# Performance work log

Hardware: AMD Instinct MI355X
Metric: run time of the kernel (lower is better)

Reference implementation:

```python
import jax, jax.numpy as jnp
import numpy as np

B, T, J, D = 1024, 128, 5, 64
H = 128            # GRU hidden
HEADS, HD = 4, 32  # GAT heads / head dim
GAT_OUT = HEADS * HD
MID, OUT, P = 128, 64, 4
NEG_SLOPE = 0.2


def setup_inputs() -> dict:
    key = jax.random.key(0)
    ks = jax.random.split(key, 20)
    s = 0.05
    obs = jax.random.normal(ks[0], (B, T, J, D), jnp.float32)
    # fixed bidirectional 5-node chain (as in _make_chain_edge_index)
    src = list(range(J - 1)) + list(range(1, J))
    dst = list(range(1, J)) + list(range(J - 1))
    edge_index = jnp.array([src, dst], dtype=jnp.int32)  # [2, 8]
    p = {
        # GRU (torch layout: gates ordered r, z, n)
        'W_ih': jax.random.normal(ks[1], (3 * H, D)) * s,
        'W_hh': jax.random.normal(ks[2], (3 * H, H)) * s,
        'b_ih': jax.random.normal(ks[3], (3 * H,)) * s,
        'b_hh': jax.random.normal(ks[4], (3 * H,)) * s,
        # GATConv
        'gat_W': jax.random.normal(ks[5], (H, GAT_OUT)) * s,
        'att_src': jax.random.normal(ks[6], (HEADS, HD)) * s,
        'att_dst': jax.random.normal(ks[7], (HEADS, HD)) * s,
        'gat_b': jax.random.normal(ks[8], (GAT_OUT,)) * s,
        # trunk MLP
        'W1': jax.random.normal(ks[9], (GAT_OUT, MID)) * s,
        'b1': jax.random.normal(ks[10], (MID,)) * s,
        'W2': jax.random.normal(ks[11], (MID, OUT)) * s,
        'b2': jax.random.normal(ks[12], (OUT,)) * s,
        # 5 actor heads stacked + critic
        'actor_W': jax.random.normal(ks[13], (J, OUT, P)) * s,
        'actor_b': jax.random.normal(ks[14], (J, P)) * s,
        'critic_W': jax.random.normal(ks[15], (OUT, 1)) * s,
        'critic_b': jax.random.normal(ks[16], (1,)) * s,
    }
    return {'obs': obs, 'edge_index': edge_index, **p}


def _forward(obs, edge_index, W_ih, W_hh, b_ih, b_hh, gat_W, att_src, att_dst,
             gat_b, W1, b1, W2, b2, actor_W, actor_b, critic_W, critic_b):
    Bb, Tt, Jj, Dd = obs.shape
    # temporal encoder: one GRU shared across junctions, batch = B*J
    x = obs.transpose(0, 2, 1, 3).reshape(Bb * Jj, Tt, Dd)

    def step(h, xt):
        gi = xt @ W_ih.T + b_ih            # [BJ, 3H]
        gh = h @ W_hh.T + b_hh
        i_r, i_z, i_n = jnp.split(gi, 3, axis=-1)
        h_r, h_z, h_n = jnp.split(gh, 3, axis=-1)
        r = jax.nn.sigmoid(i_r + h_r)
        z = jax.nn.sigmoid(i_z + h_z)
        n = jnp.tanh(i_n + r * h_n)
        return (1.0 - z) * n + z * h, None

    h0 = jnp.zeros((Bb * Jj, H), obs.dtype)
    hT, _ = jax.lax.scan(step, h0, x.transpose(1, 0, 2))  # final hidden [BJ, H]
    h = hT.reshape(Bb, Jj, H)

    # GATConv over the fixed 5-node chain, done densely per batch graph.
    # PyG semantics: edge (src -> dst), self-loops added, softmax over incoming
    # edges per dst node, messages are transformed src features.
    xp = (h @ gat_W).reshape(Bb, Jj, HEADS, HD)
    a_s = jnp.einsum('bjhd,hd->bjh', xp, att_src)  # per-src score
    a_d = jnp.einsum('bihd,hd->bih', xp, att_dst)  # per-dst score
    e = a_s[:, None, :, :] + a_d[:, :, None, :]    # [B, dst_i, src_j, heads]
    e = jax.nn.leaky_relu(e, NEG_SLOPE)
    adj = jnp.zeros((Jj, Jj), bool).at[edge_index[1], edge_index[0]].set(True)
    adj = adj | jnp.eye(Jj, dtype=bool)            # add self-loops
    e = jnp.where(adj[None, :, :, None], e, -jnp.inf)
    alpha = jax.nn.softmax(e, axis=2)              # softmax over src j per dst i
    g = jnp.einsum('bijh,bjhd->bihd', alpha, xp).reshape(Bb, Jj, GAT_OUT) + gat_b

    # shared trunk MLP
    t = jax.nn.relu(jax.nn.relu(g @ W1 + b1) @ W2 + b2)  # [B, J, OUT]

    # per-junction actor heads + critic on junction-mean
    logits = jnp.einsum('bjo,jop->bjp', t, actor_W) + actor_b  # [B, J, P]
    value = t.mean(axis=1) @ critic_W + critic_b               # [B, 1]
    return logits, value


def reference(obs, edge_index, W_ih, W_hh, b_ih, b_hh, gat_W, att_src, att_dst,
              gat_b, W1, b1, W2, b2, actor_W, actor_b, critic_W, critic_b):
    return _forward(obs, edge_index, W_ih, W_hh, b_ih, b_hh, gat_W, att_src,
                    att_dst, gat_b, W1, b1, W2, b2, actor_W, actor_b,
                    critic_W, critic_b)
```

## Files before the change

### kernel.cpp

```cpp
#include <hip/hip_runtime.h>
#include <hip/hip_bf16.h>

typedef short shortx4 __attribute__((ext_vector_type(4)));
typedef short short8 __attribute__((ext_vector_type(8)));
typedef float floatx4 __attribute__((ext_vector_type(4)));

#define MFMA_BF16(A, B, C) __builtin_amdgcn_mfma_f32_16x16x32_bf16((A), (B), (C), 0, 0, 0)
#define LOG2E 1.44269504088896340736f

__device__ __forceinline__ float bf2f(const __hip_bfloat16 v) { return __bfloat162float(v); }

__device__ __forceinline__ unsigned rne_bits(float f) {
    unsigned u = __builtin_bit_cast(unsigned, f);
    return u + 0x7fffu + ((u >> 16) & 1u);
}
__device__ __forceinline__ unsigned pack_bf16(float a, float b) {
    return (rne_bits(b) & 0xffff0000u) | (rne_bits(a) >> 16);
}
__device__ __forceinline__ short bf16_s(float f) { return (short)(rne_bits(f) >> 16); }

__device__ __forceinline__ short8 cvt8(const float4 a, const float4 b) {
    union { unsigned u[4]; short8 s; } r;
    r.u[0] = pack_bf16(a.x, a.y);
    r.u[1] = pack_bf16(a.z, a.w);
    r.u[2] = pack_bf16(b.x, b.y);
    r.u[3] = pack_bf16(b.z, b.w);
    return r.s;
}

__device__ __forceinline__ short8 ld_s8(const short* p) {
    union { struct { shortx4 lo, hi; } p; short8 v; } u;
    u.p.lo = *reinterpret_cast<const shortx4*>(p);
    u.p.hi = *reinterpret_cast<const shortx4*>(p + 4);
    return u.v;
}

__device__ __forceinline__ float fast_sigmoid(float x) {
    const float e = __builtin_amdgcn_exp2f(-x * LOG2E);
    return __builtin_amdgcn_rcpf(1.0f + e);
}
__device__ __forceinline__ float fast_tanh(float x) {
    const float e = __builtin_amdgcn_exp2f(x * (2.0f * LOG2E));
    return 1.0f - 2.0f * __builtin_amdgcn_rcpf(e + 1.0f);
}

__global__ __launch_bounds__(512) void gru_kernel(
    const float* __restrict__ obs,
    const float* __restrict__ W_ih,
    const float* __restrict__ W_hh,
    const float* __restrict__ b_ih,
    const float* __restrict__ b_hh,
    __hip_bfloat16* __restrict__ h_out)
{
    __shared__ alignas(16) short h_lds[2 * 16 * 132];
    __shared__ alignas(16) short x_lds[2 * 16 * 68];

    const int tid = threadIdx.x;
    const int w = tid >> 6;
    const int lane = tid & 63;
    const int q = lane >> 4;
    const int c = lane & 15;
    const int r0 = blockIdx.x * 16;

    for (int i = tid; i < 2 * 16 * 132; i += 512) h_lds[i] = 0;

    short8 wih[3][2];
    short8 whh[3][4];
#pragma unroll
    for (int g = 0; g < 3; ++g) {
        const int col = g * 128 + w * 16 + c;
#pragma unroll
        for (int f = 0; f < 2; ++f) {
            const float4 a = *reinterpret_cast<const float4*>(W_ih + col * 64 + f * 32 + q * 8);
            const float4 b = *reinterpret_cast<const float4*>(W_ih + col * 64 + f * 32 + q * 8 + 4);
            wih[g][f] = cvt8(a, b);
        }
#pragma unroll
        for (int f = 0; f < 4; ++f) {
            const float4 a = *reinterpret_cast<const float4*>(W_hh + col * 128 + f * 32 + q * 8);
            const float4 b = *reinterpret_cast<const float4*>(W_hh + col * 128 + f * 32 + q * 8 + 4);
            whh[g][f] = cvt8(a, b);
        }
    }

    const int cc = w * 16 + c;
    const float br_ = b_ih[cc] + b_hh[cc];
    const float bz_ = b_ih[128 + cc] + b_hh[128 + cc];
    const float bin_ = b_ih[256 + cc];
    const float bhn_ = b_hh[256 + cc];
    const floatx4 cbias_r  = {br_, br_, br_, br_};
    const floatx4 cbias_z  = {bz_, bz_, bz_, bz_};
    const floatx4 cbias_in = {bin_, bin_, bin_, bin_};
    const floatx4 cbias_hn = {bhn_, bhn_, bhn_, bhn_};

    const int srow = tid >> 5, scp = tid & 31;
    {
        const int rs = r0 + srow;
        const int bbs = rs / 5;
        const int jjs = rs - bbs * 5;
        const float* xgs = obs + bbs * 40960 + jjs * 64 + scp * 2;
        unsigned* xb32 = reinterpret_cast<unsigned*>(x_lds);
        const float2 v0 = *reinterpret_cast<const float2*>(xgs);
        xb32[srow * 34 + scp] = pack_bf16(v0.x, v0.y);
        float2 vn = *reinterpret_cast<const float2*>(xgs + 320);

        float h_keep[4] = {0.0f, 0.0f, 0.0f, 0.0f};

        __syncthreads();

        int bufo = 0;
        for (int t = 0; t < 128; ++t) {
            const int nbufo = 2112 - bufo;
            const short* hb = &h_lds[bufo];
            const short* xb = &x_lds[(t & 1) * 1088];

            const short8 xc0 = ld_s8(xb + c * 68 + q * 8);
            const short8 xc1 = ld_s8(xb + c * 68 + 32 + q * 8);
            short8 hf[4];
#pragma unroll
            for (int f = 0; f < 4; ++f)
                hf[f] = ld_s8(hb + c * 132 + f * 32 + q * 8);

            unsigned* xw = reinterpret_cast<unsigned*>(&x_lds[((t + 1) & 1) * 1088]);
            xw[srow * 34 + scp] = pack_bf16(vn.x, vn.y);
            const int tp = (t + 2) > 127 ? 127 : (t + 2);
            vn = *reinterpret_cast<const float2*>(xgs + tp * 320);

            floatx4 ar  = MFMA_BF16(xc0, wih[0][0], cbias_r);
            floatx4 az  = MFMA_BF16(xc0, wih[1][0], cbias_z);
            floatx4 ain = MFMA_BF16(xc0, wih[2][0], cbias_in);
            ar  = MFMA_BF16(xc1, wih[0][1], ar);
            az  = MFMA_BF16(xc1, wih[1][1], az);
            ain = MFMA_BF16(xc1, wih[2][1], ain);
            floatx4 ahn = MFMA_BF16(hf[0], whh[2][0], cbias_hn);
#pragma unroll
            for (int f = 0; f < 4; ++f) {
                ar = MFMA_BF16(hf[f], whh[0][f], ar);
                az = MFMA_BF16(hf[f], whh[1][f], az);
                if (f > 0) ahn = MFMA_BF16(hf[f], whh[2][f], ahn);
            }

            short* hnb = &h_lds[nbufo];
#pragma unroll
            for (int i = 0; i < 4; ++i) {
                const float rr = fast_sigmoid(ar[i]);
                const float zz = fast_sigmoid(az[i]);
                const float nn = fast_tanh(ain[i] + rr * ahn[i]);
                const float hv = nn + zz * (h_keep[i] - nn);
                h_keep[i] = hv;
                hnb[(4 * q + i) * 132 + w * 16 + c] = bf16_s(hv);
            }

            bufo = nbufo;
            __syncthreads();
        }

#pragma unroll
        for (int i = 0; i < 4; ++i)
            h_out[(r0 + 4 * q + i) * 128 + w * 16 + c] = __float2bfloat16(h_keep[i]);
    }
}

__global__ __launch_bounds__(256) void head_kernel(
    const __hip_bfloat16* __restrict__ h_in,
    const float* __restrict__ gat_W,
    const float* __restrict__ att_src,
    const float* __restrict__ att_dst,
    const float* __restrict__ gat_b,
    const float* __restrict__ W1,
    const float* __restrict__ b1,
    const float* __restrict__ W2,
    const float* __restrict__ b2,
    const float* __restrict__ actor_W,
    const float* __restrict__ actor_b,
    const float* __restrict__ critic_W,
    const float* __restrict__ critic_b,
    float* __restrict__ out)
{
    __shared__ float hs[5][128];
    __shared__ float xp[5][128];
    __shared__ float gs[5][128];
    __shared__ float t1[5][128];
    __shared__ float t2[5][64];
    __shared__ float pp[1280];
    __shared__ float as_[5][4];
    __shared__ float ad_[5][4];

    const int tid = threadIdx.x;
    const int b = blockIdx.x;

    for (int i = tid; i < 640; i += 256)
        hs[i >> 7][i & 127] = bf2f(h_in[b * 640 + i]);
    __syncthreads();

    {
        const int kh = tid >> 7, col = tid & 127;
        float acc[5] = {0, 0, 0, 0, 0};
#pragma unroll 8
        for (int k2 = 0; k2 < 64; ++k2) {
            const int k = kh * 64 + k2;
            const float wv = gat_W[k * 128 + col];
#pragma unroll
            for (int i = 0; i < 5; ++i) acc[i] += hs[i][k] * wv;
        }
#pragma unroll
        for (int i = 0; i < 5; ++i) pp[kh * 640 + i * 128 + col] = acc[i];
    }
    __syncthreads();
    for (int i = tid; i < 640; i += 256)
        xp[i >> 7][i & 127] = pp[i] + pp[640 + i];
    __syncthreads();

    if (tid < 40) {
        const int row = tid >> 3;
        const int hd = (tid >> 1) & 3;
        const int which = tid & 1;
        const float* att = which ? att_dst : att_src;
        float acc = 0.0f;
#pragma unroll
        for (int d = 0; d < 32; ++d) acc += xp[row][hd * 32 + d] * att[hd * 32 + d];
        if (which) ad_[row][hd] = acc; else as_[row][hd] = acc;
    }
    __syncthreads();

    for (int i = tid; i < 640; i += 256) {
        const int dst = i >> 7, col = i & 127, hd = col >> 5;
        const float adv = ad_[dst][hd];
        float ev[3]; int js[3]; int cnt = 0; float mx = -1e30f;
#pragma unroll
        for (int dj = -1; dj <= 1; ++dj) {
            const int j = dst + dj;
            if (j < 0 || j >= 5) continue;
            float e = as_[j][hd] + adv;
            e = e > 0.0f ? e : 0.2f * e;
            js[cnt] = j; ev[cnt] = e; mx = fmaxf(mx, e); ++cnt;
        }
        float s = 0.0f, num = 0.0f;
        for (int k = 0; k < cnt; ++k) {
            const float a = __builtin_amdgcn_exp2f((ev[k] - mx) * LOG2E);
            s += a; num += a * xp[js[k]][col];
        }
        gs[dst][col] = num * __builtin_amdgcn_rcpf(s) + gat_b[col];
    }
    __syncthreads();

    {
        const int kh = tid >> 7, col = tid & 127;
        float acc[5] = {0, 0, 0, 0, 0};
#pragma unroll 8
        for (int k2 = 0; k2 < 64; ++k2) {
            const int k = kh * 64 + k2;
            const float wv = W1[k * 128 + col];
#pragma unroll
            for (int i = 0; i < 5; ++i) acc[i] += gs[i][k] * wv;
        }
#pragma unroll
        for (int i = 0; i < 5; ++i) pp[kh * 640 + i * 128 + col] = acc[i];
    }
    __syncthreads();
    for (int i = tid; i < 640; i += 256)
        t1[i >> 7][i & 127] = fmaxf(pp[i] + pp[640 + i] + b1[i & 127], 0.0f);
    __syncthreads();

    {
        const int kq = tid >> 6, col = tid & 63;
        float acc[5] = {0, 0, 0, 0, 0};
#pragma unroll 8
        for (int k2 = 0; k2 < 32; ++k2) {
            const int k = kq * 32 + k2;
            const float wv = W2[k * 64 + col];
#pragma unroll
            for (int i = 0; i < 5; ++i) acc[i] += t1[i][k] * wv;
        }
#pragma unroll
        for (int i = 0; i < 5; ++i) pp[kq * 320 + i * 64 + col] = acc[i];
    }
    __syncthreads();
    for (int i = tid; i < 320; i += 256) {
        const int row = i >> 6, col = i & 63;
        t2[row][col] = fmaxf(pp[i] + pp[320 + i] + pp[640 + i] + pp[960 + i] + b2[col], 0.0f);
    }
    __syncthreads();

    if (tid < 20) {
        const int row = tid >> 2, p = tid & 3;
        float acc = actor_b[row * 4 + p];
#pragma unroll
        for (int o = 0; o < 64; ++o)
            acc += t2[row][o] * actor_W[row * 256 + o * 4 + p];
        out[(b * 5 + row) * 4 + p] = acc;
    }
    if (tid == 64) {
        float acc = 0.0f;
#pragma unroll
        for (int o = 0; o < 64; ++o) {
            float m = 0.0f;
#pragma unroll
            for (int j = 0; j < 5; ++j) m += t2[j][o];
            acc += (m * 0.2f) * critic_W[o];
        }
        out[20480 + b] = acc + critic_b[0];
    }
}

extern "C" void kernel_launch(void* const* d_in, const int* in_sizes, int n_in,
                              void* d_out, int out_size, void* d_ws, size_t ws_size,
                              hipStream_t stream) {
    (void)in_sizes; (void)n_in; (void)out_size; (void)ws_size;
    const float* obs      = (const float*)d_in[0];
    const float* W_ih     = (const float*)d_in[2];
    const float* W_hh     = (const float*)d_in[3];
    const float* b_ih     = (const float*)d_in[4];
    const float* b_hh     = (const float*)d_in[5];
    const float* gat_W    = (const float*)d_in[6];
    const float* att_src  = (const float*)d_in[7];
    const float* att_dst  = (const float*)d_in[8];
    const float* gat_b    = (const float*)d_in[9];
    const float* W1       = (const float*)d_in[10];
    const float* b1       = (const float*)d_in[11];
    const float* W2       = (const float*)d_in[12];
    const float* b2       = (const float*)d_in[13];
    const float* actor_W  = (const float*)d_in[14];
    const float* actor_b  = (const float*)d_in[15];
    const float* critic_W = (const float*)d_in[16];
    const float* critic_b = (const float*)d_in[17];

    __hip_bfloat16* h_ws = (__hip_bfloat16*)d_ws;

    gru_kernel<<<320, 512, 0, stream>>>(obs, W_ih, W_hh, b_ih, b_hh, h_ws);
    head_kernel<<<1024, 256, 0, stream>>>(h_ws, gat_W, att_src, att_dst, gat_b,
                                          W1, b1, W2, b2, actor_W, actor_b,
                                          critic_W, critic_b,
                                          (float*)d_out);
}
```

Baseline: 428.7 us.

## Split GRU MFMA accumulation chains and deepen obs prefetch in recurrent loop

The per-step gate accumulations are split into two independent MFMA chains per gate, summed at the end, which shortens the serial dependency through the MFMA pipeline. The global prefetch of obs is deepened from one to two steps ahead so load latency is covered across more iterations. The __syncthreads is replaced by an explicit lgkmcnt wait plus s_barrier wrapped in sched_barriers, which skips the vmcnt drain so outstanding global loads can stay in flight across the barrier. In exchange there are extra vector adds and more live registers, and the sched_barriers restrict how the compiler can reorder code.

Result: slower. 484.4 us (+13.0%).

```diff
diff --git a/kernel.cpp b/kernel.cpp
--- a/kernel.cpp
+++ b/kernel.cpp
@@ -94,71 +94,88 @@
     const floatx4 cbias_hn = {bhn_, bhn_, bhn_, bhn_};
 
     const int srow = tid >> 5, scp = tid & 31;
-    {
-        const int rs = r0 + srow;
-        const int bbs = rs / 5;
-        const int jjs = rs - bbs * 5;
-        const float* xgs = obs + bbs * 40960 + jjs * 64 + scp * 2;
-        unsigned* xb32 = reinterpret_cast<unsigned*>(x_lds);
-        const float2 v0 = *reinterpret_cast<const float2*>(xgs);
-        xb32[srow * 34 + scp] = pack_bf16(v0.x, v0.y);
-        float2 vn = *reinterpret_cast<const float2*>(xgs + 320);
-
-        float h_keep[4] = {0.0f, 0.0f, 0.0f, 0.0f};
-
-        __syncthreads();
-
-        int bufo = 0;
-        for (int t = 0; t < 128; ++t) {
-            const int nbufo = 2112 - bufo;
-            const short* hb = &h_lds[bufo];
-            const short* xb = &x_lds[(t & 1) * 1088];
-
-            const short8 xc0 = ld_s8(xb + c * 68 + q * 8);
-            const short8 xc1 = ld_s8(xb + c * 68 + 32 + q * 8);
-            short8 hf[4];
-#pragma unroll
-            for (int f = 0; f < 4; ++f)
-                hf[f] = ld_s8(hb + c * 132 + f * 32 + q * 8);
-
-            unsigned* xw = reinterpret_cast<unsigned*>(&x_lds[((t + 1) & 1) * 1088]);
-            xw[srow * 34 + scp] = pack_bf16(vn.x, vn.y);
-            const int tp = (t + 2) > 127 ? 127 : (t + 2);
-            vn = *reinterpret_cast<const float2*>(xgs + tp * 320);
-
-            floatx4 ar  = MFMA_BF16(xc0, wih[0][0], cbias_r);
-            floatx4 az  = MFMA_BF16(xc0, wih[1][0], cbias_z);
-            floatx4 ain = MFMA_BF16(xc0, wih[2][0], cbias_in);
-            ar  = MFMA_BF16(xc1, wih[0][1], ar);
-            az  = MFMA_BF16(xc1, wih[1][1], az);
-            ain = MFMA_BF16(xc1, wih[2][1], ain);
-            floatx4 ahn = MFMA_BF16(hf[0], whh[2][0], cbias_hn);
-#pragma unroll
-            for (int f = 0; f < 4; ++f) {
-                ar = MFMA_BF16(hf[f], whh[0][f], ar);
-                az = MFMA_BF16(hf[f], whh[1][f], az);
-                if (f > 0) ahn = MFMA_BF16(hf[f], whh[2][f], ahn);
-            }
-
-            short* hnb = &h_lds[nbufo];
-#pragma unroll
-            for (int i = 0; i < 4; ++i) {
-                const float rr = fast_sigmoid(ar[i]);
-                const float zz = fast_sigmoid(az[i]);
-                const float nn = fast_tanh(ain[i] + rr * ahn[i]);
-                const float hv = nn + zz * (h_keep[i] - nn);
-                h_keep[i] = hv;
-                hnb[(4 * q + i) * 132 + w * 16 + c] = bf16_s(hv);
-            }
-
-            bufo = nbufo;
-            __syncthreads();
-        }
-
-#pragma unroll
-        for (int i = 0; i < 4; ++i)
-            h_out[(r0 + 4 * q + i) * 128 + w * 16 + c] = __float2bfloat16(h_keep[i]);
-    }
+    const int rs = r0 + srow;
+    const int bbs = rs / 5;
+    const int jjs = rs - bbs * 5;
+    const float* xgs = obs + bbs * 40960 + jjs * 64 + scp * 2;
+    unsigned* xb32 = reinterpret_cast<unsigned*>(x_lds);
+
+    const float2 v0 = *reinterpret_cast<const float2*>(xgs);
+    xb32[srow * 34 + scp] = pack_bf16(v0.x, v0.y);
+    float2 vnA = *reinterpret_cast<const float2*>(xgs + 320);
+    float2 vnB = *reinterpret_cast<const float2*>(xgs + 640);
+
+    float h_keep[4] = {0.0f, 0.0f, 0.0f, 0.0f};
+
+    __syncthreads();
+
+    int bufo = 0;
+    for (int t = 0; t < 128; ++t) {
+        const int nbufo = 2112 - bufo;
+        const short* hb = &h_lds[bufo];
+        const short* xb = &x_lds[(t & 1) * 1088];
+
+        const short8 xc0 = ld_s8(xb + c * 68 + q * 8);
+        const short8 xc1 = ld_s8(xb + c * 68 + 32 + q * 8);
+        short8 hf[4];
+#pragma unroll
+        for (int f = 0; f < 4; ++f)
+            hf[f] = ld_s8(hb + c * 132 + f * 32 + q * 8);
+
+        unsigned* xw = reinterpret_cast<unsigned*>(&x_lds[((t + 1) & 1) * 1088]);
+        xw[srow * 34 + scp] = pack_bf16(vnA.x, vnA.y);
+        vnA = vnB;
+        const int tp = (t + 3 > 127) ? 127 : (t + 3);
+        vnB = *reinterpret_cast<const float2*>(xgs + tp * 320);
+
+        const floatx4 z4 = {0.0f, 0.0f, 0.0f, 0.0f};
+        floatx4 arA = MFMA_BF16(xc0, wih[0][0], cbias_r);
+        floatx4 azA = MFMA_BF16(xc0, wih[1][0], cbias_z);
+        floatx4 ain = MFMA_BF16(xc0, wih[2][0], cbias_in);
+        floatx4 arB = MFMA_BF16(xc1, wih[0][1], z4);
+        floatx4 azB = MFMA_BF16(xc1, wih[1][1], z4);
+        ain = MFMA_BF16(xc1, wih[2][1], ain);
+
+        floatx4 ahnA = MFMA_BF16(hf[0], whh[2][0], cbias_hn);
+        arA = MFMA_BF16(hf[0], whh[0][0], arA);
+        azA = MFMA_BF16(hf[0], whh[1][0], azA);
+        arA = MFMA_BF16(hf[1], whh[0][1], arA);
+        azA = MFMA_BF16(hf[1], whh[1][1], azA);
+        ahnA = MFMA_BF16(hf[1], whh[2][1], ahnA);
+
+        floatx4 ahnB = MFMA_BF16(hf[2], whh[2][2], z4);
+        arB = MFMA_BF16(hf[2], whh[0][2], arB);
+        azB = MFMA_BF16(hf[2], whh[1][2], azB);
+        arB = MFMA_BF16(hf[3], whh[0][3], arB);
+        azB = MFMA_BF16(hf[3], whh[1][3], azB);
+        ahnB = MFMA_BF16(hf[3], whh[2][3], ahnB);
+
+        const floatx4 ar  = arA + arB;
+        const floatx4 az  = azA + azB;
+        const floatx4 ahn = ahnA + ahnB;
+
+        short* hnb = &h_lds[nbufo];
+#pragma unroll
+        for (int i = 0; i < 4; ++i) {
+            const float rr = fast_sigmoid(ar[i]);
+            const float zz = fast_sigmoid(az[i]);
+            const float nn = fast_tanh(ain[i] + rr * ahn[i]);
+            const float hv = nn + zz * (h_keep[i] - nn);
+            h_keep[i] = hv;
+            hnb[(4 * q + i) * 132 + w * 16 + c] = bf16_s(hv);
+        }
+
+        bufo = nbufo;
+
+        __builtin_amdgcn_sched_barrier(0);
+        asm volatile("s_waitcnt lgkmcnt(0)" ::: "memory");
+        __builtin_amdgcn_s_barrier();
+        __builtin_amdgcn_sched_barrier(0);
+    }
+
+#pragma unroll
+    for (int i = 0; i < 4; ++i)
+        h_out[(r0 + 4 * q + i) * 128 + w * 16 + c] = __float2bfloat16(h_keep[i]);
 }
 
 __global__ __launch_bounds__(256) void head_kernel(
```

## Repartition GRU to 10-row blocks of 4 waves, each wave covering 32 hidden columns

Applied to the files above, without the earlier changes.

The GRU kernel now uses 256-thread blocks, each processing 10 sequence rows instead of 16, so 512 blocks are launched instead of 320 and every CU gets work. Each wave owns 32 hidden columns, written as two interleaved MFMA column tiles, which doubles the MFMAs per wave but halves the waves per block. The M=16 MFMA tiles are now only 10/16 utilised, and the serial per-step chain per wave gets longer, in exchange for better occupancy spread across the GPU's CUs.

Result: slower. 472.1 us (+10.1%).

```diff
diff --git a/kernel.cpp b/kernel.cpp
--- a/kernel.cpp
+++ b/kernel.cpp
@@ -17,7 +17,6 @@
 __device__ __forceinline__ unsigned pack_bf16(float a, float b) {
     return (rne_bits(b) & 0xffff0000u) | (rne_bits(a) >> 16);
 }
-__device__ __forceinline__ short bf16_s(float f) { return (short)(rne_bits(f) >> 16); }
 
 __device__ __forceinline__ short8 cvt8(const float4 a, const float4 b) {
     union { unsigned u[4]; short8 s; } r;
@@ -44,7 +43,7 @@
     return 1.0f - 2.0f * __builtin_amdgcn_rcpf(e + 1.0f);
 }
 
-__global__ __launch_bounds__(512) void gru_kernel(
+__global__ __launch_bounds__(256, 2) void gru_kernel(
     const float* __restrict__ obs,
     const float* __restrict__ W_ih,
     const float* __restrict__ W_hh,
@@ -60,104 +59,144 @@
     const int lane = tid & 63;
     const int q = lane >> 4;
     const int c = lane & 15;
-    const int r0 = blockIdx.x * 16;
-
-    for (int i = tid; i < 2 * 16 * 132; i += 512) h_lds[i] = 0;
-
-    short8 wih[3][2];
-    short8 whh[3][4];
+    const int r0 = blockIdx.x * 10;
+
+    for (int i = tid; i < 2 * 16 * 132; i += 256) h_lds[i] = 0;
+    for (int i = tid; i < 2 * 16 * 68; i += 256) x_lds[i] = 0;
+
+    short8 wih[3][2][2];
+    short8 whh[3][2][4];
 #pragma unroll
     for (int g = 0; g < 3; ++g) {
-        const int col = g * 128 + w * 16 + c;
-#pragma unroll
-        for (int f = 0; f < 2; ++f) {
-            const float4 a = *reinterpret_cast<const float4*>(W_ih + col * 64 + f * 32 + q * 8);
-            const float4 b = *reinterpret_cast<const float4*>(W_ih + col * 64 + f * 32 + q * 8 + 4);
-            wih[g][f] = cvt8(a, b);
-        }
-#pragma unroll
-        for (int f = 0; f < 4; ++f) {
-            const float4 a = *reinterpret_cast<const float4*>(W_hh + col * 128 + f * 32 + q * 8);
-            const float4 b = *reinterpret_cast<const float4*>(W_hh + col * 128 + f * 32 + q * 8 + 4);
-            whh[g][f] = cvt8(a, b);
-        }
-    }
-
-    const int cc = w * 16 + c;
-    const float br_ = b_ih[cc] + b_hh[cc];
-    const float bz_ = b_ih[128 + cc] + b_hh[128 + cc];
-    const float bin_ = b_ih[256 + cc];
-    const float bhn_ = b_hh[256 + cc];
-    const floatx4 cbias_r  = {br_, br_, br_, br_};
-    const floatx4 cbias_z  = {bz_, bz_, bz_, bz_};
-    const floatx4 cbias_in = {bin_, bin_, bin_, bin_};
-    const floatx4 cbias_hn = {bhn_, bhn_, bhn_, bhn_};
-
-    const int srow = tid >> 5, scp = tid & 31;
-    {
+#pragma unroll
+        for (int ct = 0; ct < 2; ++ct) {
+            const int col = g * 128 + w * 32 + 2 * c + ct;
+#pragma unroll
+            for (int f = 0; f < 2; ++f) {
+                const float4 a = *reinterpret_cast<const float4*>(W_ih + col * 64 + f * 32 + q * 8);
+                const float4 b = *reinterpret_cast<const float4*>(W_ih + col * 64 + f * 32 + q * 8 + 4);
+                wih[g][ct][f] = cvt8(a, b);
+            }
+#pragma unroll
+            for (int f = 0; f < 4; ++f) {
+                const float4 a = *reinterpret_cast<const float4*>(W_hh + col * 128 + f * 32 + q * 8);
+                const float4 b = *reinterpret_cast<const float4*>(W_hh + col * 128 + f * 32 + q * 8 + 4);
+                whh[g][ct][f] = cvt8(a, b);
+            }
+        }
+    }
+
+    const int c0 = w * 32 + 2 * c, c1 = c0 + 1;
+    const float br0_ = b_ih[c0] + b_hh[c0];
+    const float br1_ = b_ih[c1] + b_hh[c1];
+    const float bz0_ = b_ih[128 + c0] + b_hh[128 + c0];
+    const float bz1_ = b_ih[128 + c1] + b_hh[128 + c1];
+    const float bn0_ = b_ih[256 + c0];
+    const float bn1_ = b_ih[256 + c1];
+    const float bh0_ = b_hh[256 + c0];
+    const float bh1_ = b_hh[256 + c1];
+    const floatx4 cbr0 = {br0_, br0_, br0_, br0_};
+    const floatx4 cbr1 = {br1_, br1_, br1_, br1_};
+    const floatx4 cbz0 = {bz0_, bz0_, bz0_, bz0_};
+    const floatx4 cbz1 = {bz1_, bz1_, bz1_, bz1_};
+    const floatx4 cbn0 = {bn0_, bn0_, bn0_, bn0_};
+    const floatx4 cbn1 = {bn1_, bn1_, bn1_, bn1_};
+    const floatx4 cbh0 = {bh0_, bh0_, bh0_, bh0_};
+    const floatx4 cbh1 = {bh1_, bh1_, bh1_, bh1_};
+
+    const int srow = tid >> 4, sc = tid & 15;
+    const bool stager = (tid < 160);
+    const float* xgs = nullptr;
+    float4 vn;
+    if (stager) {
         const int rs = r0 + srow;
         const int bbs = rs / 5;
         const int jjs = rs - bbs * 5;
-        const float* xgs = obs + bbs * 40960 + jjs * 64 + scp * 2;
-        unsigned* xb32 = reinterpret_cast<unsigned*>(x_lds);
-        const float2 v0 = *reinterpret_cast<const float2*>(xgs);
-        xb32[srow * 34 + scp] = pack_bf16(v0.x, v0.y);
-        float2 vn = *reinterpret_cast<const float2*>(xgs + 320);
-
-        float h_keep[4] = {0.0f, 0.0f, 0.0f, 0.0f};
-
+        xgs = obs + bbs * 40960 + jjs * 64 + sc * 4;
+        const float4 v0 = *reinterpret_cast<const float4*>(xgs);
+        uint2* xw = reinterpret_cast<uint2*>(&x_lds[srow * 68 + sc * 4]);
+        *xw = uint2{pack_bf16(v0.x, v0.y), pack_bf16(v0.z, v0.w)};
+        vn = *reinterpret_cast<const float4*>(xgs + 320);
+    }
+
+    float hk0[4] = {0.0f, 0.0f, 0.0f, 0.0f};
+    float hk1[4] = {0.0f, 0.0f, 0.0f, 0.0f};
+
+    __syncthreads();
+
+    int bufo = 0;
+    for (int t = 0; t < 128; ++t) {
+        const int nbufo = 2112 - bufo;
+        const short* hb = &h_lds[bufo];
+        const short* xb = &x_lds[(t & 1) * 1088];
+
+        const short8 xc0 = ld_s8(xb + c * 68 + q * 8);
+        const short8 xc1 = ld_s8(xb + c * 68 + 32 + q * 8);
+        short8 hf[4];
+#pragma unroll
+        for (int f = 0; f < 4; ++f)
+            hf[f] = ld_s8(hb + c * 132 + f * 32 + q * 8);
+
+        if (stager) {
+            uint2* xw = reinterpret_cast<uint2*>(&x_lds[((t + 1) & 1) * 1088 + srow * 68 + sc * 4]);
+            *xw = uint2{pack_bf16(vn.x, vn.y), pack_bf16(vn.z, vn.w)};
+            const int tp = (t + 2) > 127 ? 127 : (t + 2);
+            vn = *reinterpret_cast<const float4*>(xgs + tp * 320);
+        }
+
+        floatx4 ar0 = MFMA_BF16(xc0, wih[0][0][0], cbr0);
+        floatx4 ar1 = MFMA_BF16(xc0, wih[0][1][0], cbr1);
+        floatx4 az0 = MFMA_BF16(xc0, wih[1][0][0], cbz0);
+        floatx4 az1 = MFMA_BF16(xc0, wih[1][1][0], cbz1);
+        floatx4 an0 = MFMA_BF16(xc0, wih[2][0][0], cbn0);
+        floatx4 an1 = MFMA_BF16(xc0, wih[2][1][0], cbn1);
+        ar0 = MFMA_BF16(xc1, wih[0][0][1], ar0);
+        ar1 = MFMA_BF16(xc1, wih[0][1][1], ar1);
+        az0 = MFMA_BF16(xc1, wih[1][0][1], az0);
+        az1 = MFMA_BF16(xc1, wih[1][1][1], az1);
+        an0 = MFMA_BF16(xc1, wih[2][0][1], an0);
+        an1 = MFMA_BF16(xc1, wih[2][1][1], an1);
+
+        floatx4 ah0 = MFMA_BF16(hf[0], whh[2][0][0], cbh0);
+        floatx4 ah1 = MFMA_BF16(hf[0], whh[2][1][0], cbh1);
+#pragma unroll
+        for (int f = 0; f < 4; ++f) {
+            ar0 = MFMA_BF16(hf[f], whh[0][0][f], ar0);
+            ar1 = MFMA_BF16(hf[f], whh[0][1][f], ar1);
+            az0 = MFMA_BF16(hf[f], whh[1][0][f], az0);
+            az1 = MFMA_BF16(hf[f], whh[1][1][f], az1);
+            if (f > 0) {
+                ah0 = MFMA_BF16(hf[f], whh[2][0][f], ah0);
+                ah1 = MFMA_BF16(hf[f], whh[2][1][f], ah1);
+            }
+        }
+
+        unsigned* hw = reinterpret_cast<unsigned*>(&h_lds[nbufo]);
+#pragma unroll
+        for (int i = 0; i < 4; ++i) {
+            const float rr0 = fast_sigmoid(ar0[i]);
+            const float rr1 = fast_sigmoid(ar1[i]);
+            const float zz0 = fast_sigmoid(az0[i]);
+            const float zz1 = fast_sigmoid(az1[i]);
+            const float nn0 = fast_tanh(an0[i] + rr0 * ah0[i]);
+            const float nn1 = fast_tanh(an1[i] + rr1 * ah1[i]);
+            const float hv0 = nn0 + zz0 * (hk0[i] - nn0);
+            const float hv1 = nn1 + zz1 * (hk1[i] - nn1);
+            hk0[i] = hv0;
+            hk1[i] = hv1;
+            hw[(4 * q + i) * 66 + w * 16 + c] = pack_bf16(hv0, hv1);
+        }
+
+        bufo = nbufo;
         __syncthreads();
-
-        int bufo = 0;
-        for (int t = 0; t < 128; ++t) {
-            const int nbufo = 2112 - bufo;
-            const short* hb = &h_lds[bufo];
-            const short* xb = &x_lds[(t & 1) * 1088];
-
-            const short8 xc0 = ld_s8(xb + c * 68 + q * 8);
-            const short8 xc1 = ld_s8(xb + c * 68 + 32 + q * 8);
-            short8 hf[4];
-#pragma unroll
-            for (int f = 0; f < 4; ++f)
-                hf[f] = ld_s8(hb + c * 132 + f * 32 + q * 8);
-
-            unsigned* xw = reinterpret_cast<unsigned*>(&x_lds[((t + 1) & 1) * 1088]);
-            xw[srow * 34 + scp] = pack_bf16(vn.x, vn.y);
-            const int tp = (t + 2) > 127 ? 127 : (t + 2);
-            vn = *reinterpret_cast<const float2*>(xgs + tp * 320);
-
-            floatx4 ar  = MFMA_BF16(xc0, wih[0][0], cbias_r);
-            floatx4 az  = MFMA_BF16(xc0, wih[1][0], cbias_z);
-            floatx4 ain = MFMA_BF16(xc0, wih[2][0], cbias_in);
-            ar  = MFMA_BF16(xc1, wih[0][1], ar);
-            az  = MFMA_BF16(xc1, wih[1][1], az);
-            ain = MFMA_BF16(xc1, wih[2][1], ain);
-            floatx4 ahn = MFMA_BF16(hf[0], whh[2][0], cbias_hn);
-#pragma unroll
-            for (int f = 0; f < 4; ++f) {
-                ar = MFMA_BF16(hf[f], whh[0][f], ar);
-                az = MFMA_BF16(hf[f], whh[1][f], az);
-                if (f > 0) ahn = MFMA_BF16(hf[f], whh[2][f], ahn);
-            }
-
-            short* hnb = &h_lds[nbufo];
-#pragma unroll
-            for (int i = 0; i < 4; ++i) {
-                const float rr = fast_sigmoid(ar[i]);
-                const float zz = fast_sigmoid(az[i]);
-                const float nn = fast_tanh(ain[i] + rr * ahn[i]);
-                const float hv = nn + zz * (h_keep[i] - nn);
-                h_keep[i] = hv;
-                hnb[(4 * q + i) * 132 + w * 16 + c] = bf16_s(hv);
-            }
-
-            bufo = nbufo;
-            __syncthreads();
-        }
-
-#pragma unroll
-        for (int i = 0; i < 4; ++i)
-            h_out[(r0 + 4 * q + i) * 128 + w * 16 + c] = __float2bfloat16(h_keep[i]);
+    }
+
+    unsigned* ho = reinterpret_cast<unsigned*>(h_out);
+#pragma unroll
+    for (int i = 0; i < 4; ++i) {
+        const int row = 4 * q + i;
+        if (row < 10)
+            ho[(r0 + row) * 64 + w * 16 + c] = pack_bf16(hk0[i], hk1[i]);
     }
 }
 
@@ -327,7 +366,7 @@
 
     __hip_bfloat16* h_ws = (__hip_bfloat16*)d_ws;
 
-    gru_kernel<<<320, 512, 0, stream>>>(obs, W_ih, W_hh, b_ih, b_hh, h_ws);
+    gru_kernel<<<512, 256, 0, stream>>>(obs, W_ih, W_hh, b_ih, b_hh, h_ws);
     head_kernel<<<1024, 256, 0, stream>>>(h_ws, gat_W, att_src, att_dst, gat_b,
                                           W1, b1, W2, b2, actor_W, actor_b,
                                           critic_W, critic_b,
```

## Rebalance GRU blocks so mixed one- and two-tile blocks fill every CU

Applied to the files above, without the earlier changes.

The GRU kernel becomes a templated body that processes one or two 16-row tiles per block. Launch drops from 320 to 256 blocks: 192 blocks take one tile and 64 blocks take two, so each CU gets one block instead of some CUs running a second round. The two-tile blocks interleave independent MFMA chains to hide the recurrence latency, at the cost of more registers and LDS and a longer per-step critical path in those blocks.

New measurement: 432.1 us. No clear change (+0.8%).

```diff
diff --git a/kernel.cpp b/kernel.cpp
--- a/kernel.cpp
+++ b/kernel.cpp
@@ -44,25 +44,27 @@
     return 1.0f - 2.0f * __builtin_amdgcn_rcpf(e + 1.0f);
 }
 
-__global__ __launch_bounds__(512) void gru_kernel(
+template<int NT>
+__device__ __forceinline__ void gru_body(
+    const int r0,
     const float* __restrict__ obs,
     const float* __restrict__ W_ih,
     const float* __restrict__ W_hh,
     const float* __restrict__ b_ih,
     const float* __restrict__ b_hh,
-    __hip_bfloat16* __restrict__ h_out)
+    __hip_bfloat16* __restrict__ h_out,
+    short* h_lds, short* x_lds)
 {
-    __shared__ alignas(16) short h_lds[2 * 16 * 132];
-    __shared__ alignas(16) short x_lds[2 * 16 * 68];
-
     const int tid = threadIdx.x;
     const int w = tid >> 6;
     const int lane = tid & 63;
     const int q = lane >> 4;
     const int c = lane & 15;
-    const int r0 = blockIdx.x * 16;
-
-    for (int i = tid; i < 2 * 16 * 132; i += 512) h_lds[i] = 0;
+
+    constexpr int HBUF = NT * 16 * 132;
+    constexpr int XBUF = NT * 16 * 68;
+
+    for (int i = tid; i < 2 * HBUF; i += 512) h_lds[i] = 0;
 
     short8 wih[3][2];
     short8 whh[3][4];
@@ -93,72 +95,132 @@
     const floatx4 cbias_in = {bin_, bin_, bin_, bin_};
     const floatx4 cbias_hn = {bhn_, bhn_, bhn_, bhn_};
 
-    const int srow = tid >> 5, scp = tid & 31;
+    int srow, scw;
+    const float* xgs;
+    float2 vn2;
+    float4 vn4;
+    if constexpr (NT == 1) {
+        srow = tid >> 5; scw = tid & 31;
+    } else {
+        srow = tid >> 4; scw = tid & 15;
+    }
     {
         const int rs = r0 + srow;
         const int bbs = rs / 5;
         const int jjs = rs - bbs * 5;
-        const float* xgs = obs + bbs * 40960 + jjs * 64 + scp * 2;
-        unsigned* xb32 = reinterpret_cast<unsigned*>(x_lds);
-        const float2 v0 = *reinterpret_cast<const float2*>(xgs);
-        xb32[srow * 34 + scp] = pack_bf16(v0.x, v0.y);
-        float2 vn = *reinterpret_cast<const float2*>(xgs + 320);
-
-        float h_keep[4] = {0.0f, 0.0f, 0.0f, 0.0f};
-
+        if constexpr (NT == 1) {
+            xgs = obs + bbs * 40960 + jjs * 64 + scw * 2;
+            const float2 v0 = *reinterpret_cast<const float2*>(xgs);
+            reinterpret_cast<unsigned*>(x_lds)[srow * 34 + scw] = pack_bf16(v0.x, v0.y);
+            vn2 = *reinterpret_cast<const float2*>(xgs + 320);
+        } else {
+            xgs = obs + bbs * 40960 + jjs * 64 + scw * 4;
+            const float4 v0 = *reinterpret_cast<const float4*>(xgs);
+            *reinterpret_cast<uint2*>(&x_lds[srow * 68 + scw * 4]) =
+                uint2{pack_bf16(v0.x, v0.y), pack_bf16(v0.z, v0.w)};
+            vn4 = *reinterpret_cast<const float4*>(xgs + 320);
+        }
+    }
+
+    float hk[NT][4] = {};
+
+    __syncthreads();
+
+    int bufo = 0;
+    for (int t = 0; t < 128; ++t) {
+        const int nbufo = HBUF - bufo;
+        const short* hb = &h_lds[bufo];
+        const short* xb = &x_lds[(t & 1) * XBUF];
+
+        short8 xc0[NT], xc1[NT], hf[NT][4];
+#pragma unroll
+        for (int T = 0; T < NT; ++T) {
+            const short* xr = xb + (T * 16 + c) * 68;
+            xc0[T] = ld_s8(xr + q * 8);
+            xc1[T] = ld_s8(xr + 32 + q * 8);
+            const short* hr = hb + (T * 16 + c) * 132;
+#pragma unroll
+            for (int f = 0; f < 4; ++f)
+                hf[T][f] = ld_s8(hr + f * 32 + q * 8);
+        }
+
+        const int tp = (t + 2) > 127 ? 127 : (t + 2);
+        if constexpr (NT == 1) {
+            unsigned* xw = reinterpret_cast<unsigned*>(&x_lds[((t + 1) & 1) * XBUF]);
+            xw[srow * 34 + scw] = pack_bf16(vn2.x, vn2.y);
+            vn2 = *reinterpret_cast<const float2*>(xgs + tp * 320);
+        } else {
+            *reinterpret_cast<uint2*>(&x_lds[((t + 1) & 1) * XBUF + srow * 68 + scw * 4]) =
+                uint2{pack_bf16(vn4.x, vn4.y), pack_bf16(vn4.z, vn4.w)};
+            vn4 = *reinterpret_cast<const float4*>(xgs + tp * 320);
+        }
+
+        floatx4 ar[NT], az[NT], an[NT], ah[NT];
+#pragma unroll
+        for (int T = 0; T < NT; ++T) {
+            ar[T] = MFMA_BF16(xc0[T], wih[0][0], cbias_r);
+            az[T] = MFMA_BF16(xc0[T], wih[1][0], cbias_z);
+            an[T] = MFMA_BF16(xc0[T], wih[2][0], cbias_in);
+        }
+#pragma unroll
+        for (int T = 0; T < NT; ++T) {
+            ar[T] = MFMA_BF16(xc1[T], wih[0][1], ar[T]);
+            az[T] = MFMA_BF16(xc1[T], wih[1][1], az[T]);
+            an[T] = MFMA_BF16(xc1[T], wih[2][1], an[T]);
+            ah[T] = MFMA_BF16(hf[T][0], whh[2][0], cbias_hn);
+        }
+#pragma unroll
+        for (int f = 0; f < 4; ++f) {
+#pragma unroll
+            for (int T = 0; T < NT; ++T) {
+                ar[T] = MFMA_BF16(hf[T][f], whh[0][f], ar[T]);
+                az[T] = MFMA_BF16(hf[T][f], whh[1][f], az[T]);
+                if (f > 0) ah[T] = MFMA_BF16(hf[T][f], whh[2][f], ah[T]);
+            }
+        }
+
+        short* hnb = &h_lds[nbufo];
+#pragma unroll
+        for (int T = 0; T < NT; ++T) {
+#pragma unroll
+            for (int i = 0; i < 4; ++i) {
+                const float rr = fast_sigmoid(ar[T][i]);
+                const float zz = fast_sigmoid(az[T][i]);
+                const float nn = fast_tanh(an[T][i] + rr * ah[T][i]);
+                const float hv = nn + zz * (hk[T][i] - nn);
+                hk[T][i] = hv;
+                hnb[(T * 16 + 4 * q + i) * 132 + w * 16 + c] = bf16_s(hv);
+            }
+        }
+
+        bufo = nbufo;
         __syncthreads();
-
-        int bufo = 0;
-        for (int t = 0; t < 128; ++t) {
-            const int nbufo = 2112 - bufo;
-            const short* hb = &h_lds[bufo];
-            const short* xb = &x_lds[(t & 1) * 1088];
-
-            const short8 xc0 = ld_s8(xb + c * 68 + q * 8);
-            const short8 xc1 = ld_s8(xb + c * 68 + 32 + q * 8);
-            short8 hf[4];
-#pragma unroll
-            for (int f = 0; f < 4; ++f)
-                hf[f] = ld_s8(hb + c * 132 + f * 32 + q * 8);
-
-            unsigned* xw = reinterpret_cast<unsigned*>(&x_lds[((t + 1) & 1) * 1088]);
-            xw[srow * 34 + scp] = pack_bf16(vn.x, vn.y);
-            const int tp = (t + 2) > 127 ? 127 : (t + 2);
-            vn = *reinterpret_cast<const float2*>(xgs + tp * 320);
-
-            floatx4 ar  = MFMA_BF16(xc0, wih[0][0], cbias_r);
-            floatx4 az  = MFMA_BF16(xc0, wih[1][0], cbias_z);
-            floatx4 ain = MFMA_BF16(xc0, wih[2][0], cbias_in);
-            ar  = MFMA_BF16(xc1, wih[0][1], ar);
-            az  = MFMA_BF16(xc1, wih[1][1], az);
-            ain = MFMA_BF16(xc1, wih[2][1], ain);
-            floatx4 ahn = MFMA_BF16(hf[0], whh[2][0], cbias_hn);
-#pragma unroll
-            for (int f = 0; f < 4; ++f) {
-                ar = MFMA_BF16(hf[f], whh[0][f], ar);
-                az = MFMA_BF16(hf[f], whh[1][f], az);
-                if (f > 0) ahn = MFMA_BF16(hf[f], whh[2][f], ahn);
-            }
-
-            short* hnb = &h_lds[nbufo];
-#pragma unroll
-            for (int i = 0; i < 4; ++i) {
-                const float rr = fast_sigmoid(ar[i]);
-                const float zz = fast_sigmoid(az[i]);
-                const float nn = fast_tanh(ain[i] + rr * ahn[i]);
-                const float hv = nn + zz * (h_keep[i] - nn);
-                h_keep[i] = hv;
-                hnb[(4 * q + i) * 132 + w * 16 + c] = bf16_s(hv);
-            }
-
-            bufo = nbufo;
-            __syncthreads();
-        }
-
+    }
+
+#pragma unroll
+    for (int T = 0; T < NT; ++T)
 #pragma unroll
         for (int i = 0; i < 4; ++i)
-            h_out[(r0 + 4 * q + i) * 128 + w * 16 + c] = __float2bfloat16(h_keep[i]);
-    }
+            h_out[(r0 + T * 16 + 4 * q + i) * 128 + w * 16 + c] = __float2bfloat16(hk[T][i]);
+}
+
+__global__ __launch_bounds__(512, 2) void gru_kernel(
+    const float* __restrict__ obs,
+    const float* __restrict__ W_ih,
+    const float* __restrict__ W_hh,
+    const float* __restrict__ b_ih,
+    const float* __restrict__ b_hh,
+    __hip_bfloat16* __restrict__ h_out)
+{
+    __shared__ alignas(16) short h_lds[2 * 32 * 132];
+    __shared__ alignas(16) short x_lds[2 * 32 * 68];
+
+    const int bid = blockIdx.x;
+    if (bid < 192)
+        gru_body<1>(bid * 16, obs, W_ih, W_hh, b_ih, b_hh, h_out, h_lds, x_lds);
+    else
+        gru_body<2>(3072 + (bid - 192) * 32, obs, W_ih, W_hh, b_ih, b_hh, h_out,
+                    h_lds, x_lds);
 }
 
 __global__ __launch_bounds__(256) void head_kernel(
@@ -327,7 +389,7 @@
 
     __hip_bfloat16* h_ws = (__hip_bfloat16*)d_ws;
 
-    gru_kernel<<<320, 512, 0, stream>>>(obs, W_ih, W_hh, b_ih, b_hh, h_ws);
+    gru_kernel<<<256, 512, 0, stream>>>(obs, W_ih, W_hh, b_ih, b_hh, h_ws);
     head_kernel<<<1024, 256, 0, stream>>>(h_ws, gat_W, att_src, att_dst, gat_b,
                                           W1, b1, W2, b2, actor_W, actor_b,
                                           critic_W, critic_b,
```
